# Kernel tuning notes

Measured on AMD Instinct MI355X. Metric: run time of the kernel, lower is better.

The kernel has to match this reference:

```python
import jax, jax.numpy as jnp
import numpy as np

B, T, C = 1, 2048, 2048
H, G, D = 16, 4, 128   # n_head, n_query_groups, head_size
I = 8192               # intermediate_size


def _hv(x, alpha, beta):
    # ParamHeaveside forward: alpha * heaviside(x - beta)
    return (alpha * (x - beta > 0).astype(x.dtype)).astype(x.dtype)


def _normed_linear(x, w, scale):
    # NormedLinear: column-center then L2-normalize columns (dim=0), scaled
    w = w - w.mean(axis=0, keepdims=True)
    n = jnp.maximum(jnp.sqrt((w * w).sum(axis=0, keepdims=True)), 1e-12)
    return x @ (scale * w / n).T


def _rope(t, cos, sin):
    # non-interleaved rotary (rotate-half), cos/sin: [T, D/2]
    half = t.shape[-1] // 2
    t1, t2 = t[..., :half], t[..., half:]
    c, s = cos[None, :, None, :], sin[None, :, None, :]
    return jnp.concatenate([t1 * c - t2 * s, t1 * s + t2 * c], axis=-1)


def _block(x, cos, sin, attn_w, proj_w, proj_scale, fc_w, mlp_proj_w, mlp_proj_scale,
           in_alpha, in_beta, q_alpha, q_beta, k_alpha, k_beta,
           out_alpha, out_beta, act1_alpha, act1_beta, act2_alpha, act2_beta, hv):
    q_per_kv = H // G
    h = hv(x, in_alpha, in_beta)                      # encoder_input (norm is identity)
    qkv = (h @ attn_w.T).reshape(B, T, G, q_per_kv + 2, D)
    q = qkv[:, :, :, :q_per_kv, :].reshape(B, T, H, D)
    k = qkv[:, :, :, q_per_kv, :]                     # [B,T,G,D]
    v = qkv[:, :, :, q_per_kv + 1, :]                 # [B,T,G,D]
    q = hv(_rope(q, cos, sin), q_alpha, q_beta)
    k = hv(_rope(k, cos, sin), k_alpha, k_beta)
    q = q.transpose(0, 2, 1, 3)                       # [B,H,T,D]
    k = jnp.repeat(k.transpose(0, 2, 1, 3), q_per_kv, axis=1)
    v = jnp.repeat(v.transpose(0, 2, 1, 3), q_per_kv, axis=1)
    scores = jnp.einsum('bhtd,bhsd->bhts', q, k) * (1.0 / D)  # scale = 1/head_size
    causal = jnp.tril(jnp.ones((T, T), bool))
    w = jnp.where(causal[None, None], jax.nn.relu(scores), 0.0)  # relu-attention
    y = jnp.einsum('bhts,bhsd->bhtd', w, v).transpose(0, 2, 1, 3).reshape(B, T, C)
    y = _normed_linear(hv(y, out_alpha, out_beta), proj_w, proj_scale)
    x = x + y
    m = hv(x, act1_alpha, act1_beta) @ fc_w.T
    m = _normed_linear(hv(m, act2_alpha, act2_beta), mlp_proj_w, mlp_proj_scale)
    return x + m


def setup_inputs() -> dict:
    key = jax.random.key(0)
    ks = jax.random.split(key, 8)
    rn = lambda k, s, sc=0.02: (jax.random.normal(k, s) * sc).astype(jnp.float32)
    theta = 1.0 / (10000.0 ** (jnp.arange(0, D, 2, dtype=jnp.float32) / D))
    idx = jnp.outer(jnp.arange(T, dtype=jnp.float32), theta)
    return {
        'x': jax.random.normal(ks[0], (B, T, C), dtype=jnp.float32),
        'cos': jnp.cos(idx), 'sin': jnp.sin(idx),
        'attn_w': rn(ks[1], ((H + 2 * G) * D, C)),
        'proj_w': rn(ks[2], (C, C)), 'proj_scale': jnp.float32(0.01),
        'fc_w': rn(ks[3], (I, C)),
        'mlp_proj_w': rn(ks[4], (C, I)), 'mlp_proj_scale': jnp.float32(0.01),
        'in_alpha': jnp.full((C,), 0.5, jnp.float32), 'in_beta': rn(ks[5], (C,), 0.01),
        'q_alpha': jnp.full((D,), 0.5, jnp.float32), 'q_beta': jnp.zeros((D,), jnp.float32),
        'k_alpha': jnp.full((D,), 0.5, jnp.float32), 'k_beta': jnp.zeros((D,), jnp.float32),
        'out_alpha': jnp.full((C,), 0.5, jnp.float32), 'out_beta': rn(ks[6], (C,), 0.01),
        'act1_alpha': jnp.full((C,), 0.5, jnp.float32), 'act1_beta': rn(ks[7], (C,), 0.01),
        'act2_alpha': jnp.full((I,), 0.5, jnp.float32), 'act2_beta': jnp.zeros((I,), jnp.float32),
    }


def reference(x, cos, sin, attn_w, proj_w, proj_scale, fc_w, mlp_proj_w, mlp_proj_scale,
              in_alpha, in_beta, q_alpha, q_beta, k_alpha, k_beta,
              out_alpha, out_beta, act1_alpha, act1_beta, act2_alpha, act2_beta):
    return _block(x, cos, sin, attn_w, proj_w, proj_scale, fc_w, mlp_proj_w, mlp_proj_scale,
                  in_alpha, in_beta, q_alpha, q_beta, k_alpha, k_beta,
                  out_alpha, out_beta, act1_alpha, act1_beta, act2_alpha, act2_beta, _hv)
```

## Files before the change

### kernel.cpp

```cpp
#include <hip/hip_runtime.h>

typedef __attribute__((ext_vector_type(8))) short short8;
typedef __attribute__((ext_vector_type(4))) float f32x4;
typedef __attribute__((ext_vector_type(4))) int i32x4;

constexpr int TT = 2048, CC = 2048, HQ = 16, GG = 4, DD = 128, IC = 8192;

__device__ __forceinline__ ushort f2b(float f) {
  union { float f; unsigned u; } v; v.f = f;
  unsigned r = v.u + 0x7fffu + ((v.u >> 16) & 1u);
  return (ushort)(r >> 16);
}
__device__ __forceinline__ float b2f(ushort u) {
  union { unsigned u; float f; } v; v.u = ((unsigned)u) << 16; return v.f;
}
__device__ __forceinline__ char q8(float eff, float r) {
  float q = rintf(eff * r);
  q = fminf(fmaxf(q, -127.f), 127.f);
  return (char)(int)q;
}

__device__ __forceinline__ void gload16(const void* g, void* l) {
  __builtin_amdgcn_global_load_lds(
      (const __attribute__((address_space(1))) void*)g,
      (__attribute__((address_space(3))) void*)l, 16, 0, 0);
}

#define BAR()    __builtin_amdgcn_s_barrier()
#define PRIO1()  __builtin_amdgcn_s_setprio(1)
#define PRIO0()  __builtin_amdgcn_s_setprio(0)

template<int EPI>
__global__ __launch_bounds__(512, 2)
void gemm_i8(const char* __restrict__ A, const char* __restrict__ B,
             void* __restrict__ C0, const float* __restrict__ s,
             const float* __restrict__ beta, int M, int N, int K, int kc)
{
  __shared__ alignas(16) char lds[131072];
  const int tid = threadIdx.x;
  const int l = tid & 63, w = tid >> 6;
  const int fl = l & 15, fh = l >> 4;
  const int wrm = w >> 2, wcn = w & 3;
  const int m0 = blockIdx.y * 256, n0 = blockIdx.x * 256;
  const int kBeg = blockIdx.z * kc;
  const int kEnd = (kBeg + kc < K) ? kBeg + kc : K;
  const int nt = (kEnd - kBeg) >> 7;

  i32x4 acc[8][4] = {};

  const int srow = tid >> 3;
  const int scol = ((tid & 7) ^ (srow & 7)) * 16;
  const char* Ag = A + (size_t)(m0 + srow) * K + kBeg + scol;
  const char* Bg = B + (size_t)(n0 + srow) * K + kBeg + scol;

  auto stage_half = [&](int tile, int h) {
    const char* base = (h < 2) ? Ag : Bg;
    const int half = h & 1;
    const char* g = base + (size_t)(half * 128) * K + tile * 128;
    char* d = lds + (tile & 1) * 65536 + ((h < 2) ? 0 : 32768) + half * 16384 + tid * 16;
    gload16(g, d);
    gload16(g + (size_t)64 * K, d + 8192);
  };

  auto readA = [&](i32x4 (&dst)[4][2], int buf, int mofs) {
#pragma unroll
    for (int mf = 0; mf < 4; ++mf)
#pragma unroll
      for (int ks = 0; ks < 2; ++ks) {
        int row = wrm * 128 + (mofs + mf) * 16 + fl;
        dst[mf][ks] = *(const i32x4*)(lds + buf * 65536 + row * 128 +
                                      (((ks * 4 + fh) ^ (row & 7)) * 16));
      }
  };
  auto readB = [&](i32x4 (&dst)[2][2], int buf, int nofs) {
#pragma unroll
    for (int nf = 0; nf < 2; ++nf)
#pragma unroll
      for (int ks = 0; ks < 2; ++ks) {
        int row = wcn * 64 + (nofs + nf) * 16 + fl;
        dst[nf][ks] = *(const i32x4*)(lds + buf * 65536 + 32768 + row * 128 +
                                      (((ks * 4 + fh) ^ (row & 7)) * 16));
      }
  };
  auto mmQ = [&](i32x4 (&a)[4][2], i32x4 (&b)[2][2], int mo, int no) {
    PRIO1();
#pragma unroll
    for (int mf = 0; mf < 4; ++mf)
#pragma unroll
      for (int nf = 0; nf < 2; ++nf)
#pragma unroll
        for (int ks = 0; ks < 2; ++ks)
          acc[mo + mf][no + nf] = __builtin_amdgcn_mfma_i32_16x16x64_i8(
              a[mf][ks], b[nf][ks], acc[mo + mf][no + nf], 0, 0, 0);
    PRIO0();
  };

  stage_half(0, 0); stage_half(0, 1); stage_half(0, 2); stage_half(0, 3);
  if (nt > 1) {
    stage_half(1, 2); stage_half(1, 3);
    asm volatile("s_waitcnt vmcnt(4)" ::: "memory");
  } else {
    asm volatile("s_waitcnt vmcnt(0)" ::: "memory");
  }
  BAR();

  for (int t = 0; t < nt; ++t) {
    const int buf = t & 1;
    i32x4 A0[4][2], A1[4][2], B0[2][2], B1[2][2];

    readA(A0, buf, 0);
    readB(B0, buf, 0);
    if (t + 1 < nt) stage_half(t + 1, 0);
    BAR();
    mmQ(A0, B0, 0, 0);

    readB(B1, buf, 2);
    if (t + 1 < nt) stage_half(t + 1, 1);
    BAR();
    mmQ(A0, B1, 0, 2);

    readA(A1, buf, 4);
    BAR();
    mmQ(A1, B0, 4, 0);

    if (t + 2 < nt) { stage_half(t + 2, 2); stage_half(t + 2, 3); }
    if (t <= nt - 3) asm volatile("s_waitcnt vmcnt(4)" ::: "memory");
    else             asm volatile("s_waitcnt vmcnt(0)" ::: "memory");
    BAR();
    mmQ(A1, B1, 4, 2);
  }

  const int orow0 = m0 + wrm * 128 + fh * 4;
  const int ocol0 = n0 + wcn * 64 + fl;
#pragma unroll
  for (int mf = 0; mf < 8; ++mf) {
#pragma unroll
    for (int nf = 0; nf < 4; ++nf) {
      const int c = ocol0 + nf * 16;
      const float sc = s[c];
#pragma unroll
      for (int j = 0; j < 4; ++j) {
        const int r = orow0 + mf * 16 + j;
        const size_t o = (size_t)r * N + c;
        float v = (float)acc[mf][nf][j] * sc;
        if constexpr (EPI == 1) {
          ((char*)C0)[o] = (v - beta[c] > 0.f) ? (char)1 : (char)0;
        } else {
          ((ushort*)C0 + (size_t)blockIdx.z * M * N)[o] = f2b(v);
        }
      }
    }
  }
}

template<int NS, int MODE>
__global__ void reduce_kernel(const ushort* p0, const ushort* p1, const ushort* p2, const ushort* p3,
                              const float* resid, float* outf, char* outb,
                              const float* beta, int n4, int cols)
{
  const ushort* ps[4] = {p0, p1, p2, p3};
  for (int i = blockIdx.x * blockDim.x + threadIdx.x; i < n4; i += gridDim.x * blockDim.x) {
    float4 s = ((const float4*)resid)[i];
#pragma unroll
    for (int z = 0; z < NS; ++z) {
      ushort4 q = ((const ushort4*)ps[z])[i];
      s.x += b2f(q.x); s.y += b2f(q.y); s.z += b2f(q.z); s.w += b2f(q.w);
    }
    ((float4*)outf)[i] = s;
    if constexpr (MODE == 1) {
      int c = (i * 4) & (cols - 1);
      char4 r;
      r.x = (s.x - beta[c] > 0.f) ? 1 : 0;
      r.y = (s.y - beta[c + 1] > 0.f) ? 1 : 0;
      r.z = (s.z - beta[c + 2] > 0.f) ? 1 : 0;
      r.w = (s.w - beta[c + 3] > 0.f) ? 1 : 0;
      ((char4*)outb)[i] = r;
    }
  }
}

__global__ __launch_bounds__(256)
void attn_kernel(const ushort* __restrict__ qb, const ushort* __restrict__ kb,
                 const ushort* __restrict__ vt, char* __restrict__ hy,
                 const float* __restrict__ obeta)
{
  __shared__ alignas(16) ushort Ks[2][64 * 128];
  __shared__ alignas(16) ushort Vs[2][128 * 64];
  __shared__ alignas(16) ushort Ps[64 * 64];
  const int bx = blockIdx.x;
  const int h = blockIdx.y;
  const int qi = (h & 8) ? bx : (31 - bx);
  const int g = h >> 2;
  const int q0 = qi * 64;
  const int tid = threadIdx.x;
  const int w = tid >> 6, l = tid & 63;
  const int fl = l & 15, fh = l >> 4;

  auto stageK = [&](int buf, int s0t) {
#pragma unroll
    for (int i = 0; i < 4; ++i) {
      int row = w * 16 + i * 4 + (l >> 4);
      int c16 = (l & 15) ^ (row & 7);
      gload16(kb + (size_t)g * TT * DD + (size_t)(s0t + row) * DD + c16 * 8,
              (char*)Ks[buf] + (w << 12) + (i << 10) + (l << 4));
    }
  };
  auto stageV = [&](int buf, int s0t) {
#pragma unroll
    for (int i = 0; i < 4; ++i) {
      int d = w * 32 + i * 8 + (l >> 3);
      int c16 = (l & 7) ^ (d & 7);
      gload16(vt + (size_t)g * DD * TT + (size_t)d * TT + s0t + c16 * 8,
              (char*)Vs[buf] + (w << 12) + (i << 10) + (l << 4));
    }
  };

  short8 qf[4];
  {
    const ushort* qp = qb + (size_t)h * TT * DD + (size_t)(q0 + w * 16 + fl) * DD + fh * 8;
#pragma unroll
    for (int ks = 0; ks < 4; ++ks) qf[ks] = *(const short8*)(qp + ks * 32);
  }

  stageK(0, 0); stageV(0, 0);
  asm volatile("s_waitcnt vmcnt(0)" ::: "memory");
  BAR();

  f32x4 oacc[8] = {};
  int buf = 0;

  for (int s0 = 0; s0 <= q0; s0 += 64) {
    const bool more = (s0 + 64 <= q0);
    if (more) { stageK(buf ^ 1, s0 + 64); stageV(buf ^ 1, s0 + 64); }

    f32x4 sacc[4] = {};
#pragma unroll
    for (int ks = 0; ks < 4; ++ks) {
#pragma unroll
      for (int n = 0; n < 4; ++n) {
        int krow = n * 16 + fl;
        int slotB = (ks * 4 + fh) ^ (krow & 7);
        short8 b = *(const short8*)((char*)Ks[buf] + krow * 256 + slotB * 16);
        sacc[n] = __builtin_amdgcn_mfma_f32_16x16x32_bf16(qf[ks], b, sacc[n], 0, 0, 0);
      }
    }

#pragma unroll
    for (int n = 0; n < 4; ++n) {
      const int scol = s0 + n * 16 + fl;
#pragma unroll
      for (int j = 0; j < 4; ++j) {
        const int pr = w * 16 + fh * 4 + j;
        const int qr = q0 + pr;
        float v = sacc[n][j] * 0.0078125f;
        ushort pv = (scol <= qr && v > 0.f) ? f2b(v) : (ushort)0;
        int slot = ((n * 2) + (fl >> 3)) ^ (pr & 7);
        ((ushort*)((char*)Ps + pr * 128 + slot * 16))[fl & 7] = pv;
      }
    }

    const int prow = w * 16 + fl;
#pragma unroll
    for (int ks = 0; ks < 2; ++ks) {
      int slotA = (ks * 4 + fh) ^ (prow & 7);
      short8 pa = *(const short8*)((char*)Ps + prow * 128 + slotA * 16);
#pragma unroll
      for (int n = 0; n < 8; ++n) {
        int vrow = n * 16 + fl;
        int slotB = (ks * 4 + fh) ^ (vrow & 7);
        short8 vb = *(const short8*)((char*)Vs[buf] + vrow * 128 + slotB * 16);
        oacc[n] = __builtin_amdgcn_mfma_f32_16x16x32_bf16(pa, vb, oacc[n], 0, 0, 0);
      }
    }

    if (more) {
      asm volatile("s_waitcnt vmcnt(0)" ::: "memory");
      BAR();
      buf ^= 1;
    }
  }

#pragma unroll
  for (int n = 0; n < 8; ++n) {
    const int c = h * DD + n * 16 + fl;
    const float be = obeta[c];
#pragma unroll
    for (int j = 0; j < 4; ++j) {
      const int tq = q0 + w * 16 + fh * 4 + j;
      float v = oacc[n][j];
      hy[(size_t)tq * CC + c] = (v - be > 0.f) ? (char)1 : (char)0;
    }
  }
}

__global__ __launch_bounds__(256)
void rope_hv_kernel(const ushort* __restrict__ qp0, const ushort* __restrict__ qp1,
                    const float* __restrict__ cs, const float* __restrict__ sn,
                    const float* __restrict__ qalpha, const float* __restrict__ qbeta,
                    const float* __restrict__ kalpha, const float* __restrict__ kbeta,
                    ushort* __restrict__ qb, ushort* __restrict__ kb,
                    ushort* __restrict__ vt)
{
  __shared__ ushort Vsh[64][129];
  const int t0 = blockIdx.x * 64, g = blockIdx.y, job = blockIdx.z;
  const int tid = threadIdx.x;
  if (job < 5) {
    const int hh = job;
    const float* alpha = (hh < 4) ? qalpha : kalpha;
    const float* beta = (hh < 4) ? qbeta : kbeta;
    const int hoff = (hh < 4) ? hh * 128 : 512;
    for (int it = 0; it < 16; ++it) {
      int idx = it * 256 + tid;
      int tr = idx >> 6, dd = idx & 63;
      size_t base = (size_t)(t0 + tr) * 3072 + g * 768 + hoff;
      float x1 = b2f(qp0[base + dd]) + b2f(qp1[base + dd]);
      float x2 = b2f(qp0[base + 64 + dd]) + b2f(qp1[base + 64 + dd]);
      float c = cs[(size_t)(t0 + tr) * 64 + dd];
      float s = sn[(size_t)(t0 + tr) * 64 + dd];
      float o1 = x1 * c - x2 * s, o2 = x1 * s + x2 * c;
      ushort b1 = (o1 - beta[dd] > 0.f) ? f2b(alpha[dd]) : (ushort)0;
      ushort b2 = (o2 - beta[64 + dd] > 0.f) ? f2b(alpha[64 + dd]) : (ushort)0;
      if (hh < 4) {
        size_t o = ((size_t)(g * 4 + hh) * TT + t0 + tr) * DD;
        qb[o + dd] = b1;
        qb[o + 64 + dd] = b2;
      } else {
        size_t o = ((size_t)g * TT + t0 + tr) * DD;
        kb[o + dd] = b1;
        kb[o + 64 + dd] = b2;
      }
    }
  } else {
    for (int it = 0; it < 32; ++it) {
      int idx = it * 256 + tid;
      int tr = idx >> 7, d = idx & 127;
      size_t src = (size_t)(t0 + tr) * 3072 + g * 768 + 640 + d;
      Vsh[tr][d] = f2b(b2f(qp0[src]) + b2f(qp1[src]));
    }
    __syncthreads();
    for (int it = 0; it < 32; ++it) {
      int idx = it * 256 + tid;
      int d = idx >> 6, tl = idx & 63;
      vt[((size_t)g * DD + d) * TT + t0 + tl] = Vsh[tl][d];
    }
  }
}

__global__ __launch_bounds__(256)
void quant_fused(const float* __restrict__ attn_w, char* __restrict__ attn_q,
                 const float* __restrict__ fc_w, char* __restrict__ fc_q,
                 const float* __restrict__ proj_w, char* __restrict__ proj_q,
                 const float* __restrict__ mlp_w, char* __restrict__ mlp_q,
                 const float* __restrict__ inA, const float* __restrict__ a1A,
                 const float* __restrict__ pmu, const float* __restrict__ pinv,
                 const float* __restrict__ outA,
                 const float* __restrict__ mmu, const float* __restrict__ minv,
                 const float* __restrict__ a2A,
                 float* __restrict__ s_all,
                 const float* __restrict__ x, const float* __restrict__ ib,
                 char* __restrict__ h_in)
{
  __shared__ float wmax[4];
  const int bx = blockIdx.x;
  const int tid = threadIdx.x;
  const int wv = tid >> 6, lane = tid & 63;

  if (bx < 3328) {
    const float* W; char* Q; const float4* A4;
    const float4* MU4 = nullptr; const float4* INV4 = nullptr;
    int row, sofs;
    if (bx < 768)       { W = attn_w; Q = attn_q; A4 = (const float4*)inA;  row = bx * 4 + wv;          sofs = 0; }
    else if (bx < 2816) { W = fc_w;   Q = fc_q;   A4 = (const float4*)a1A;  row = (bx - 768) * 4 + wv;  sofs = 3072; }
    else                { W = proj_w; Q = proj_q; A4 = (const float4*)outA; row = (bx - 2816) * 4 + wv; sofs = 11264;
                          MU4 = (const float4*)pmu; INV4 = (const float4*)pinv; }
    const float4* src = (const float4*)(W + (size_t)row * 2048);
    char4* dst = (char4*)(Q + (size_t)row * 2048);
    float4 ef[8];
    float m = 0.f;
#pragma unroll
    for (int it = 0; it < 8; ++it) {
      int i = it * 64 + lane;
      float4 v = src[i];
      float4 a = A4[i];
      float4 e;
      if (MU4) {
        float4 mu = MU4[i], iv = INV4[i];
        e.x = (v.x - mu.x) * iv.x * a.x;
        e.y = (v.y - mu.y) * iv.y * a.y;
        e.z = (v.z - mu.z) * iv.z * a.z;
        e.w = (v.w - mu.w) * iv.w * a.w;
      } else {
        e.x = v.x * a.x; e.y = v.y * a.y; e.z = v.z * a.z; e.w = v.w * a.w;
      }
      ef[it] = e;
      m = fmaxf(m, fmaxf(fmaxf(fabsf(e.x), fabsf(e.y)), fmaxf(fabsf(e.z), fabsf(e.w))));
    }
    for (int mask = 32; mask; mask >>= 1) m = fmaxf(m, __shfl_xor(m, mask));
    if (lane == 0) s_all[sofs + row] = m * (1.f / 127.f);
    const float r = (m > 0.f) ? 127.f / m : 0.f;
#pragma unroll
    for (int it = 0; it < 8; ++it) {
      int i = it * 64 + lane;
      char4 q;
      q.x = q8(ef[it].x, r); q.y = q8(ef[it].y, r);
      q.z = q8(ef[it].z, r); q.w = q8(ef[it].w, r);
      dst[i] = q;
    }
  } else if (bx < 5376) {
    const int row = bx - 3328;
    const float4* src = (const float4*)(mlp_w + (size_t)row * 8192);
    const float4* MU4 = (const float4*)mmu;
    const float4* INV4 = (const float4*)minv;
    const float4* A4 = (const float4*)a2A;
    char4* dst = (char4*)(mlp_q + (size_t)row * 8192);
    float4 ef[8];
    float m = 0.f;
#pragma unroll
    for (int it = 0; it < 8; ++it) {
      int i = wv * 512 + it * 64 + lane;
      float4 v = src[i];
      float4 mu = MU4[i], iv = INV4[i], a = A4[i];
      float4 e;
      e.x = (v.x - mu.x) * iv.x * a.x;
      e.y = (v.y - mu.y) * iv.y * a.y;
      e.z = (v.z - mu.z) * iv.z * a.z;
      e.w = (v.w - mu.w) * iv.w * a.w;
      ef[it] = e;
      m = fmaxf(m, fmaxf(fmaxf(fabsf(e.x), fabsf(e.y)), fmaxf(fabsf(e.z), fabsf(e.w))));
    }
    for (int mask = 32; mask; mask >>= 1) m = fmaxf(m, __shfl_xor(m, mask));
    if (lane == 0) wmax[wv] = m;
    __syncthreads();
    m = fmaxf(fmaxf(wmax[0], wmax[1]), fmaxf(wmax[2], wmax[3]));
    if (tid == 0) s_all[13312 + row] = m * (1.f / 127.f);
    const float r = (m > 0.f) ? 127.f / m : 0.f;
#pragma unroll
    for (int it = 0; it < 8; ++it) {
      int i = wv * 512 + it * 64 + lane;
      char4 q;
      q.x = q8(ef[it].x, r); q.y = q8(ef[it].y, r);
      q.z = q8(ef[it].z, r); q.w = q8(ef[it].w, r);
      dst[i] = q;
    }
  } else {
    const int blk = bx - 5376;
    const int stride = 512 * 256;
    const float4* ib4 = (const float4*)ib;
    for (int i = blk * 256 + tid; i < 2048 * 2048 / 4; i += stride) {
      float4 v = ((const float4*)x)[i];
      float4 b = ib4[i & 511];
      char4 q;
      q.x = (v.x - b.x > 0.f) ? 1 : 0;
      q.y = (v.y - b.y > 0.f) ? 1 : 0;
      q.z = (v.z - b.z > 0.f) ? 1 : 0;
      q.w = (v.w - b.w > 0.f) ? 1 : 0;
      ((char4*)h_in)[i] = q;
    }
  }
}

__global__ void stats1_all(const float* __restrict__ pw, const float* __restrict__ mw,
                           float* __restrict__ ps, float* __restrict__ ps2,
                           float* __restrict__ ms, float* __restrict__ ms2)
{
  const int bx = blockIdx.x, chunk = blockIdx.y;
  const float* W;
  float* os; float* os2; int cols, j;
  if (bx < 8) { W = pw; os = ps; os2 = ps2; cols = 2048; j = bx * 256 + threadIdx.x; }
  else        { W = mw; os = ms; os2 = ms2; cols = 8192; j = (bx - 8) * 256 + threadIdx.x; }
  const float* p = W + (size_t)chunk * 128 * cols + j;
  float s = 0.f, s2 = 0.f;
  for (int i = 0; i < 128; ++i) { float v = p[(size_t)i * cols]; s += v; s2 += v * v; }
  os[chunk * cols + j] = s;
  os2[chunk * cols + j] = s2;
}

__global__ void stats2_all(const float* __restrict__ ps, const float* __restrict__ ps2,
                           float* __restrict__ p_mu, float* __restrict__ p_inv,
                           const float* __restrict__ pscale,
                           const float* __restrict__ ms, const float* __restrict__ ms2,
                           float* __restrict__ m_mu, float* __restrict__ m_inv,
                           const float* __restrict__ mscale)
{
  const int bx = blockIdx.x;
  const float* S; const float* S2; float* mu; float* inv; const float* sc; int cols, j;
  if (bx < 8) { S = ps; S2 = ps2; mu = p_mu; inv = p_inv; sc = pscale; cols = 2048; j = bx * 256 + threadIdx.x; }
  else        { S = ms; S2 = ms2; mu = m_mu; inv = m_inv; sc = mscale; cols = 8192; j = (bx - 8) * 256 + threadIdx.x; }
  float s = 0.f, s2 = 0.f;
  for (int c = 0; c < 16; ++c) { s += S[c * cols + j]; s2 += S2[c * cols + j]; }
  float m = s * (1.f / 2048.f);
  float var = s2 - s * m;
  float nn = sqrtf(fmaxf(var, 0.f));
  nn = fmaxf(nn, 1e-12f);
  mu[j] = m;
  inv[j] = sc[0] / nn;
}

extern "C" void kernel_launch(void* const* d_in, const int* in_sizes, int n_in,
                              void* d_out, int out_size, void* d_ws, size_t ws_size,
                              hipStream_t stream) {
  const float* x          = (const float*)d_in[0];
  const float* cosT       = (const float*)d_in[1];
  const float* sinT       = (const float*)d_in[2];
  const float* attn_w     = (const float*)d_in[3];
  const float* proj_w     = (const float*)d_in[4];
  const float* proj_scale = (const float*)d_in[5];
  const float* fc_w       = (const float*)d_in[6];
  const float* mlp_proj_w = (const float*)d_in[7];
  const float* mlp_scale  = (const float*)d_in[8];
  const float* in_alpha   = (const float*)d_in[9];
  const float* in_beta    = (const float*)d_in[10];
  const float* q_alpha    = (const float*)d_in[11];
  const float* q_beta     = (const float*)d_in[12];
  const float* k_alpha    = (const float*)d_in[13];
  const float* k_beta     = (const float*)d_in[14];
  const float* out_alpha  = (const float*)d_in[15];
  const float* out_beta   = (const float*)d_in[16];
  const float* act1_alpha = (const float*)d_in[17];
  const float* act1_beta  = (const float*)d_in[18];
  const float* act2_alpha = (const float*)d_in[19];
  const float* act2_beta  = (const float*)d_in[20];

  char* cur = (char*)d_ws;
  auto alloc = [&](size_t b) { void* p = cur; cur += (b + 255) & ~(size_t)255; return p; };

  char* attn_q = (char*)alloc((size_t)3072 * 2048);
  char* fc_q   = (char*)alloc((size_t)8192 * 2048);
  char* proj_q = (char*)alloc((size_t)2048 * 2048);
  char* mlp_q  = (char*)alloc((size_t)2048 * 8192);
  char* h_in   = (char*)alloc((size_t)2048 * 2048);
  char* h_y    = (char*)alloc((size_t)2048 * 2048);
  char* h2     = (char*)alloc((size_t)2048 * 2048);
  char* h3     = (char*)alloc((size_t)2048 * 8192);
  ushort* qbuf  = (ushort*)alloc((size_t)HQ * TT * DD * 2);
  ushort* kbuf  = (ushort*)alloc((size_t)GG * TT * DD * 2);
  ushort* vtbuf = (ushort*)alloc((size_t)GG * DD * TT * 2);
  float* x2 = (float*)alloc((size_t)2048 * 2048 * 4);
  ushort* qkv_parts  = (ushort*)alloc((size_t)2 * 2048 * 3072 * 2);
  ushort* proj_parts = (ushort*)alloc((size_t)4 * 2048 * 2048 * 2);
  ushort* mlp_parts  = (ushort*)alloc((size_t)4 * 2048 * 2048 * 2);
  float* pp_s  = (float*)alloc(16 * 2048 * 4);
  float* pp_s2 = (float*)alloc(16 * 2048 * 4);
  float* mp_s  = (float*)alloc(16 * 8192 * 4);
  float* mp_s2 = (float*)alloc(16 * 8192 * 4);
  float* p_mu  = (float*)alloc(2048 * 4);
  float* p_inv = (float*)alloc(2048 * 4);
  float* m_mu  = (float*)alloc(8192 * 4);
  float* m_inv = (float*)alloc(8192 * 4);
  float* s_all = (float*)alloc(15360 * 4);

  const size_t PLANE_QKV = (size_t)2048 * 3072;
  const size_t PLANE     = (size_t)2048 * 2048;

  float* s_attn = s_all;
  float* s_fc   = s_all + 3072;
  float* s_proj = s_all + 11264;
  float* s_mlp  = s_all + 13312;

  stats1_all<<<dim3(40, 16), 256, 0, stream>>>(proj_w, mlp_proj_w, pp_s, pp_s2, mp_s, mp_s2);
  stats2_all<<<40, 256, 0, stream>>>(pp_s, pp_s2, p_mu, p_inv, proj_scale,
                                     mp_s, mp_s2, m_mu, m_inv, mlp_scale);
  quant_fused<<<5888, 256, 0, stream>>>(attn_w, attn_q, fc_w, fc_q, proj_w, proj_q,
                                        mlp_proj_w, mlp_q,
                                        in_alpha, act1_alpha, p_mu, p_inv, out_alpha,
                                        m_mu, m_inv, act2_alpha, s_all,
                                        x, in_beta, h_in);

  gemm_i8<3><<<dim3(3072 / 256, 2048 / 256, 2), 512, 0, stream>>>(
      h_in, attn_q, qkv_parts, s_attn, nullptr, 2048, 3072, 2048, 1024);

  rope_hv_kernel<<<dim3(TT / 64, GG, 6), 256, 0, stream>>>(
      qkv_parts, qkv_parts + PLANE_QKV, cosT, sinT,
      q_alpha, q_beta, k_alpha, k_beta, qbuf, kbuf, vtbuf);

  attn_kernel<<<dim3(TT / 64, HQ), 256, 0, stream>>>(qbuf, kbuf, vtbuf, h_y, out_beta);

  gemm_i8<3><<<dim3(2048 / 256, 2048 / 256, 4), 512, 0, stream>>>(
      h_y, proj_q, proj_parts, s_proj, nullptr, 2048, 2048, 2048, 512);
  reduce_kernel<4, 1><<<2048, 256, 0, stream>>>(
      proj_parts, proj_parts + PLANE, proj_parts + 2 * PLANE, proj_parts + 3 * PLANE,
      x, x2, h2, act1_beta, 2048 * 2048 / 4, 2048);

  gemm_i8<1><<<dim3(8192 / 256, 2048 / 256, 1), 512, 0, stream>>>(
      h2, fc_q, h3, s_fc, act2_beta, 2048, 8192, 2048, 2048);

  gemm_i8<3><<<dim3(8, 8, 4), 512, 0, stream>>>(
      h3, mlp_q, mlp_parts, s_mlp, nullptr, 2048, 2048, 8192, 2048);
  reduce_kernel<4, 2><<<2048, 256, 0, stream>>>(
      mlp_parts, mlp_parts + PLANE, mlp_parts + 2 * PLANE, mlp_parts + 3 * PLANE,
      x2, (float*)d_out, nullptr, nullptr, 2048 * 2048 / 4, 1);
}
```

Baseline: 274.4 us.

## Single-buffer attention K/V tiles and skip causal mask on off-diagonal tiles

Replaces the double-buffered K/V staging in the relu-attention kernel with a single buffer that is loaded, waited on, and barriered at the top of each iteration. A trailing barrier is added so the buffer is not overwritten while still being read. This halves K/V LDS use, which may allow more resident blocks, but gives up overlap of global loads with MFMA compute. It also adds a mask-free P-write path for off-diagonal tiles, where the causal check is always true.

```diff
diff --git a/kernel.cpp b/kernel.cpp
--- a/kernel.cpp
+++ b/kernel.cpp
@@ -184,8 +184,8 @@
                  const ushort* __restrict__ vt, char* __restrict__ hy,
                  const float* __restrict__ obeta)
 {
-  __shared__ alignas(16) ushort Ks[2][64 * 128];
-  __shared__ alignas(16) ushort Vs[2][128 * 64];
+  __shared__ alignas(16) ushort Ks[64 * 128];
+  __shared__ alignas(16) ushort Vs[128 * 64];
   __shared__ alignas(16) ushort Ps[64 * 64];
   const int bx = blockIdx.x;
   const int h = blockIdx.y;
@@ -196,22 +196,22 @@
   const int w = tid >> 6, l = tid & 63;
   const int fl = l & 15, fh = l >> 4;
 
-  auto stageK = [&](int buf, int s0t) {
+  auto stageK = [&](int s0t) {
 #pragma unroll
     for (int i = 0; i < 4; ++i) {
       int row = w * 16 + i * 4 + (l >> 4);
       int c16 = (l & 15) ^ (row & 7);
       gload16(kb + (size_t)g * TT * DD + (size_t)(s0t + row) * DD + c16 * 8,
-              (char*)Ks[buf] + (w << 12) + (i << 10) + (l << 4));
+              (char*)Ks + (w << 12) + (i << 10) + (l << 4));
     }
   };
-  auto stageV = [&](int buf, int s0t) {
+  auto stageV = [&](int s0t) {
 #pragma unroll
     for (int i = 0; i < 4; ++i) {
       int d = w * 32 + i * 8 + (l >> 3);
       int c16 = (l & 7) ^ (d & 7);
       gload16(vt + (size_t)g * DD * TT + (size_t)d * TT + s0t + c16 * 8,
-              (char*)Vs[buf] + (w << 12) + (i << 10) + (l << 4));
+              (char*)Vs + (w << 12) + (i << 10) + (l << 4));
     }
   };
 
@@ -222,16 +222,12 @@
     for (int ks = 0; ks < 4; ++ks) qf[ks] = *(const short8*)(qp + ks * 32);
   }
 
-  stageK(0, 0); stageV(0, 0);
-  asm volatile("s_waitcnt vmcnt(0)" ::: "memory");
-  BAR();
-
   f32x4 oacc[8] = {};
-  int buf = 0;
 
   for (int s0 = 0; s0 <= q0; s0 += 64) {
-    const bool more = (s0 + 64 <= q0);
-    if (more) { stageK(buf ^ 1, s0 + 64); stageV(buf ^ 1, s0 + 64); }
+    stageK(s0); stageV(s0);
+    asm volatile("s_waitcnt vmcnt(0)" ::: "memory");
+    BAR();
 
     f32x4 sacc[4] = {};
 #pragma unroll
@@ -240,22 +236,36 @@
       for (int n = 0; n < 4; ++n) {
         int krow = n * 16 + fl;
         int slotB = (ks * 4 + fh) ^ (krow & 7);
-        short8 b = *(const short8*)((char*)Ks[buf] + krow * 256 + slotB * 16);
+        short8 b = *(const short8*)((char*)Ks + krow * 256 + slotB * 16);
         sacc[n] = __builtin_amdgcn_mfma_f32_16x16x32_bf16(qf[ks], b, sacc[n], 0, 0, 0);
       }
     }
 
-#pragma unroll
-    for (int n = 0; n < 4; ++n) {
-      const int scol = s0 + n * 16 + fl;
-#pragma unroll
-      for (int j = 0; j < 4; ++j) {
-        const int pr = w * 16 + fh * 4 + j;
-        const int qr = q0 + pr;
-        float v = sacc[n][j] * 0.0078125f;
-        ushort pv = (scol <= qr && v > 0.f) ? f2b(v) : (ushort)0;
-        int slot = ((n * 2) + (fl >> 3)) ^ (pr & 7);
-        ((ushort*)((char*)Ps + pr * 128 + slot * 16))[fl & 7] = pv;
+    if (s0 == q0) {
+#pragma unroll
+      for (int n = 0; n < 4; ++n) {
+        const int scol = s0 + n * 16 + fl;
+#pragma unroll
+        for (int j = 0; j < 4; ++j) {
+          const int pr = w * 16 + fh * 4 + j;
+          const int qr = q0 + pr;
+          float v = sacc[n][j] * 0.0078125f;
+          ushort pv = (scol <= qr && v > 0.f) ? f2b(v) : (ushort)0;
+          int slot = ((n * 2) + (fl >> 3)) ^ (pr & 7);
+          ((ushort*)((char*)Ps + pr * 128 + slot * 16))[fl & 7] = pv;
+        }
+      }
+    } else {
+#pragma unroll
+      for (int n = 0; n < 4; ++n) {
+#pragma unroll
+        for (int j = 0; j < 4; ++j) {
+          const int pr = w * 16 + fh * 4 + j;
+          float v = sacc[n][j] * 0.0078125f;
+          ushort pv = (v > 0.f) ? f2b(v) : (ushort)0;
+          int slot = ((n * 2) + (fl >> 3)) ^ (pr & 7);
+          ((ushort*)((char*)Ps + pr * 128 + slot * 16))[fl & 7] = pv;
+        }
       }
     }
 
@@ -268,16 +278,12 @@
       for (int n = 0; n < 8; ++n) {
         int vrow = n * 16 + fl;
         int slotB = (ks * 4 + fh) ^ (vrow & 7);
-        short8 vb = *(const short8*)((char*)Vs[buf] + vrow * 128 + slotB * 16);
+        short8 vb = *(const short8*)((char*)Vs + vrow * 128 + slotB * 16);
         oacc[n] = __builtin_amdgcn_mfma_f32_16x16x32_bf16(pa, vb, oacc[n], 0, 0, 0);
       }
     }
 
-    if (more) {
-      asm volatile("s_waitcnt vmcnt(0)" ::: "memory");
-      BAR();
-      buf ^= 1;
-    }
+    BAR();
   }
 
 #pragma unroll
```

Measured after the change: 268.8 us. 2.1% less time.
